# Kernel optimization log

Hardware: AMD Instinct MI355X
Metric: run time of the kernel (lower is better)

The kernel has to match this reference:

```python
import jax, jax.numpy as jnp
import numpy as np

B, S, D = 8, 2048, 512

def setup_inputs() -> dict:
    key = jax.random.key(0)
    ks = jax.random.split(key, 9)
    scale = 1.0 / np.sqrt(D)
    return {
        "x": jax.random.normal(ks[0], (B, S, D), dtype=jnp.float32),
        "attention_mask": jax.random.uniform(ks[1], (B, S), dtype=jnp.float32),
        "Wq": jax.random.normal(ks[2], (D, D), dtype=jnp.float32) * scale,
        "bq": jax.random.normal(ks[3], (D,), dtype=jnp.float32) * 0.01,
        "Wk": jax.random.normal(ks[4], (D, D), dtype=jnp.float32) * scale,
        "bk": jax.random.normal(ks[5], (D,), dtype=jnp.float32) * 0.01,
        "Wv": jax.random.normal(ks[6], (D, D), dtype=jnp.float32) * scale,
        "bv": jax.random.normal(ks[7], (D,), dtype=jnp.float32) * 0.01,
    }

def reference(x, attention_mask, Wq, bq, Wk, bk, Wv, bv):
    # Single-head self-attention, full O(S^2) scores as in the original.
    q = jnp.einsum('bsd,df->bsf', x, Wq) + bq  # [B,S,D]
    k = jnp.einsum('bsd,df->bsf', x, Wk) + bk
    v = jnp.einsum('bsd,df->bsf', x, Wv) + bv
    scores = jnp.einsum('bqd,bkd->bqk', q, k) / jnp.sqrt(jnp.float32(D))  # [B,S,S]
    attn = jax.nn.softmax(scores, axis=2)
    weighted = jnp.einsum('bqk,bkd->bqd', attn, v)  # [B,S,D]
    # mask applied multiplicatively to the output, per original code
    return weighted * attention_mask[:, :, None]
```

## Files before the change

### kernel.cpp

```cpp
#include <hip/hip_runtime.h>
#include <math.h>
#include <stdint.h>


typedef _Float16 f16x8 __attribute__((ext_vector_type(8)));
typedef _Float16 f16x4 __attribute__((ext_vector_type(4)));
typedef _Float16 f16x2 __attribute__((ext_vector_type(2)));
typedef float f32x4 __attribute__((ext_vector_type(4)));

__device__ __forceinline__ void async16(const _Float16* g, _Float16* l) {
    __builtin_amdgcn_global_load_lds(
        (const __attribute__((address_space(1))) unsigned int*)(uintptr_t)g,
        (__attribute__((address_space(3))) unsigned int*)(unsigned int)(uintptr_t)l,
        16, 0, 0);
}

__device__ __forceinline__ float frag_sum8(f16x8 v, float acc) {
#if __has_builtin(__builtin_amdgcn_fdot2)
    const f16x2 one2 = {(_Float16)1.f, (_Float16)1.f};
    const f16x2* p = (const f16x2*)&v;
    acc = __builtin_amdgcn_fdot2(p[0], one2, acc, false);
    acc = __builtin_amdgcn_fdot2(p[1], one2, acc, false);
    acc = __builtin_amdgcn_fdot2(p[2], one2, acc, false);
    acc = __builtin_amdgcn_fdot2(p[3], one2, acc, false);
#else
#pragma unroll
    for (int j = 0; j < 8; j++) acc += (float)v[j];
#endif
    return acc;
}

template <bool WITH_RS>
__device__ __forceinline__ void core8(
    const _Float16* __restrict__ A,
    const _Float16* __restrict__ B,
    int ld, int K, int row0, int col0,
    _Float16* sm, f32x4 acc[4][4], float rs[4])
{
    constexpr int CA = 32, L = 6, BUFH = 24576;
    const int tid = threadIdx.x, lane = tid & 63, wave = tid >> 6;
    const int wm = wave >> 1, wn = wave & 1;
    const int rc  = lane >> 3;
    const int swz = ((lane & 7) ^ rc) * 8;
    const int fr = lane & 15, q = lane >> 4, fx = fr & 7;

    const _Float16* g[L];
    int coff[L];
#pragma unroll
    for (int i = 0; i < L; i++) {
        int c = wave * L + i;
        const _Float16* base = (c < CA) ? A : B;
        int rr = (c < CA) ? (row0 + 8 * c) : (col0 + 8 * (c - CA));
        g[i]    = base + (size_t)(rr + rc) * ld + swz;
        coff[i] = c * 512;
    }

    const int NT = K >> 6;
#pragma unroll
    for (int i = 0; i < L; i++) async16(g[i], sm + coff[i]);
#pragma unroll
    for (int i = 0; i < L; i++) async16(g[i] + 64, sm + BUFH + coff[i]);
#pragma unroll
    for (int i = 0; i < L; i++) g[i] += 128;
    asm volatile("s_waitcnt vmcnt(6)" ::: "memory");
    asm volatile("" ::: "memory");
    __builtin_amdgcn_s_barrier();
    asm volatile("" ::: "memory");

#pragma unroll 2
    for (int t = 0; t < NT; ++t) {
        const _Float16* As = sm + (t & 1) * BUFH;
        const _Float16* Bs = As + CA * 512;
        f16x8 ah[2][2], b0[2][2], b1[2][2];

#pragma unroll
        for (int m = 0; m < 2; m++)
#pragma unroll
            for (int s = 0; s < 2; s++) {
                int ra = (wm * 4 + m) * 16 + fr;
                int kc = ((s * 4 + q) ^ fx) * 8;
                ah[m][s] = *(const f16x8*)&As[ra * 64 + kc];
            }
#pragma unroll
        for (int n = 0; n < 2; n++)
#pragma unroll
            for (int s = 0; s < 2; s++) {
                int rb = (wn * 4 + n) * 16 + fr;
                int kc = ((s * 4 + q) ^ fx) * 8;
                b0[n][s] = *(const f16x8*)&Bs[rb * 64 + kc];
            }
        if (WITH_RS) {
#pragma unroll
            for (int m = 0; m < 2; m++)
#pragma unroll
                for (int s = 0; s < 2; s++) rs[m] = frag_sum8(ah[m][s], rs[m]);
        }
        __builtin_amdgcn_s_setprio(1);
#pragma unroll
        for (int m = 0; m < 2; m++)
#pragma unroll
            for (int n = 0; n < 2; n++)
#pragma unroll
                for (int s = 0; s < 2; s++)
                    acc[m][n] = __builtin_amdgcn_mfma_f32_16x16x32_f16(
                        ah[m][s], b0[n][s], acc[m][n], 0, 0, 0);
        __builtin_amdgcn_s_setprio(0);

#pragma unroll
        for (int n = 0; n < 2; n++)
#pragma unroll
            for (int s = 0; s < 2; s++) {
                int rb = (wn * 4 + 2 + n) * 16 + fr;
                int kc = ((s * 4 + q) ^ fx) * 8;
                b1[n][s] = *(const f16x8*)&Bs[rb * 64 + kc];
            }
        __builtin_amdgcn_s_setprio(1);
#pragma unroll
        for (int m = 0; m < 2; m++)
#pragma unroll
            for (int n = 0; n < 2; n++)
#pragma unroll
                for (int s = 0; s < 2; s++)
                    acc[m][2 + n] = __builtin_amdgcn_mfma_f32_16x16x32_f16(
                        ah[m][s], b1[n][s], acc[m][2 + n], 0, 0, 0);
        __builtin_amdgcn_s_setprio(0);

#pragma unroll
        for (int m = 0; m < 2; m++)
#pragma unroll
            for (int s = 0; s < 2; s++) {
                int ra = (wm * 4 + 2 + m) * 16 + fr;
                int kc = ((s * 4 + q) ^ fx) * 8;
                ah[m][s] = *(const f16x8*)&As[ra * 64 + kc];
            }
        if (WITH_RS) {
#pragma unroll
            for (int m = 0; m < 2; m++)
#pragma unroll
                for (int s = 0; s < 2; s++) rs[2 + m] = frag_sum8(ah[m][s], rs[2 + m]);
        }
        __builtin_amdgcn_s_setprio(1);
#pragma unroll
        for (int m = 0; m < 2; m++)
#pragma unroll
            for (int n = 0; n < 2; n++)
#pragma unroll
                for (int s = 0; s < 2; s++)
                    acc[2 + m][2 + n] = __builtin_amdgcn_mfma_f32_16x16x32_f16(
                        ah[m][s], b1[n][s], acc[2 + m][2 + n], 0, 0, 0);
        __builtin_amdgcn_s_setprio(0);

        asm volatile("s_waitcnt lgkmcnt(0)" ::: "memory");
        asm volatile("" ::: "memory");
        __builtin_amdgcn_s_barrier();
        asm volatile("" ::: "memory");
        if (t + 2 < NT) {
            _Float16* db = sm + (t & 1) * BUFH;
#pragma unroll
            for (int i = 0; i < L; i++) async16(g[i], db + coff[i]);
#pragma unroll
            for (int i = 0; i < L; i++) g[i] += 64;
        }
        __builtin_amdgcn_s_setprio(1);
#pragma unroll
        for (int m = 0; m < 2; m++)
#pragma unroll
            for (int n = 0; n < 2; n++)
#pragma unroll
                for (int s = 0; s < 2; s++)
                    acc[2 + m][n] = __builtin_amdgcn_mfma_f32_16x16x32_f16(
                        ah[m][s], b0[n][s], acc[2 + m][n], 0, 0, 0);
        __builtin_amdgcn_s_setprio(0);
        if (t + 2 < NT) {
            asm volatile("s_waitcnt vmcnt(6)" ::: "memory");
        } else if (t + 1 < NT) {
            asm volatile("s_waitcnt vmcnt(0)" ::: "memory");
        }
        if (t + 1 < NT) {
            asm volatile("" ::: "memory");
            __builtin_amdgcn_s_barrier();
            asm volatile("" ::: "memory");
        }
    }
}

__global__ __launch_bounds__(256) void prep(
    const float* __restrict__ x,
    const float* __restrict__ Wq, const float* __restrict__ Wk,
    const float* __restrict__ Wv,
    _Float16* __restrict__ Xh,
    _Float16* __restrict__ WqT, _Float16* __restrict__ WkT,
    _Float16* __restrict__ WvT)
{
    const int bid = blockIdx.x;
    if (bid < 8192) {
        int i = (bid * 256 + threadIdx.x) * 4;
        float4 v = *(const float4*)(x + i);
        f16x4 h;
        h.x = (_Float16)v.x; h.y = (_Float16)v.y;
        h.z = (_Float16)v.z; h.w = (_Float16)v.w;
        *(f16x4*)&Xh[i] = h;
    } else {
        int t = bid - 8192;
        int z = t >> 10;
        const float* W = (z == 0) ? Wq : (z == 1) ? Wk : Wv;
        _Float16* Wt   = (z == 0) ? WqT : (z == 1) ? WkT : WvT;
        int idx = (t & 1023) * 256 + threadIdx.x;
        int n = idx >> 9, k = idx & 511;
        Wt[idx] = (_Float16)W[k * 512 + n];
    }
}

__global__ __launch_bounds__(512, 2) void proj_mfma(
    const _Float16* __restrict__ Xh,
    const _Float16* __restrict__ WqT, const float* __restrict__ bq,
    const _Float16* __restrict__ WkT, const float* __restrict__ bk,
    const _Float16* __restrict__ WvT, const float* __restrict__ bv,
    _Float16* __restrict__ Qh, _Float16* __restrict__ Kh,
    _Float16* __restrict__ Vt)
{
    __shared__ __align__(16) _Float16 smem[2 * 24576];

    const int z = blockIdx.z;
    f32x4 acc[4][4];
#pragma unroll
    for (int i = 0; i < 4; i++)
#pragma unroll
        for (int j = 0; j < 4; j++) acc[i][j] = (f32x4){0.f, 0.f, 0.f, 0.f};
    float rs_unused[4];

    const int lane = threadIdx.x & 63, wave = threadIdx.x >> 6;
    const int wm = wave >> 1, wn = wave & 1;
    const int er = (lane >> 4) * 4, ec = lane & 15;

    if (z < 2) {
        const _Float16* Wt = (z == 0) ? WqT : WkT;
        const float* bias  = (z == 0) ? bq : bk;
        _Float16* P        = (z == 0) ? Qh : Kh;
        const float sc     = (z == 0) ? 0.04419417382415922f : 1.0f;
        const int row0 = blockIdx.x * 256, col0 = blockIdx.y * 128;
        core8<false>(Xh, Wt, 512, 512, row0, col0, smem, acc, rs_unused);
#pragma unroll
        for (int mf = 0; mf < 4; mf++)
#pragma unroll
            for (int nf = 0; nf < 4; nf++) {
                int col = col0 + (wn * 4 + nf) * 16 + ec;
                float bb = bias[col];
#pragma unroll
                for (int r = 0; r < 4; r++) {
                    int row = row0 + (wm * 4 + mf) * 16 + er + r;
                    P[(size_t)row * 512 + col] = (_Float16)((acc[mf][nf][r] + bb) * sc);
                }
            }
    } else {
        const int idx = blockIdx.y * 64 + blockIdx.x;
        const int row0 = (idx >> 7) * 256;
        const int col0 = (idx & 127) * 128;
        core8<false>(WvT, Xh, 512, 512, row0, col0, smem, acc, rs_unused);
#pragma unroll
        for (int mf = 0; mf < 4; mf++)
#pragma unroll
            for (int nf = 0; nf < 4; nf++) {
                int col = col0 + (wn * 4 + nf) * 16 + ec;
                size_t obase = (size_t)(col >> 11) * (512 * 2048) + (col & 2047);
#pragma unroll
                for (int r = 0; r < 4; r++) {
                    int row = row0 + (wm * 4 + mf) * 16 + er + r;
                    Vt[obase + (size_t)row * 2048] = (_Float16)(acc[mf][nf][r] + bv[row]);
                }
            }
    }
}

__global__ __launch_bounds__(512, 2) void scores_mfma(
    const _Float16* __restrict__ Qh, const _Float16* __restrict__ Kh,
    _Float16* __restrict__ Sh)
{
    __shared__ __align__(16) _Float16 smem[2 * 24576];
    const int bid = blockIdx.x;
    const int b   = bid & 7;
    const int rem = bid >> 3;
    const int col0 = (rem & 15) * 128;
    const int row0 = (rem >> 4) * 256;

    const _Float16* A = Qh + (size_t)b * 2048 * 512;
    const _Float16* B = Kh + (size_t)b * 2048 * 512;
    _Float16* S = Sh + (size_t)b * 2048 * 2048;

    f32x4 acc[4][4];
#pragma unroll
    for (int i = 0; i < 4; i++)
#pragma unroll
        for (int j = 0; j < 4; j++) acc[i][j] = (f32x4){0.f, 0.f, 0.f, 0.f};
    float rs_unused[4];

    core8<false>(A, B, 512, 512, row0, col0, smem, acc, rs_unused);

    const int lane = threadIdx.x & 63, wave = threadIdx.x >> 6;
    const int wm = wave >> 1, wn = wave & 1;
    const int er = (lane >> 4) * 4, ec = lane & 15;
#pragma unroll
    for (int mf = 0; mf < 4; mf++)
#pragma unroll
        for (int nf = 0; nf < 4; nf++) {
            int col = col0 + (wn * 4 + nf) * 16 + ec;
#pragma unroll
            for (int r = 0; r < 4; r++) {
                int row = row0 + (wm * 4 + mf) * 16 + er + r;
                S[(size_t)row * 2048 + col] = (_Float16)__expf(acc[mf][nf][r]);
            }
        }
}

__global__ __launch_bounds__(512, 2) void av_mfma(
    const _Float16* __restrict__ Sh, const _Float16* __restrict__ Vt,
    const float* __restrict__ mask, float* __restrict__ out)
{
    __shared__ __align__(16) _Float16 smem[2 * 24576];
    const int bid = blockIdx.x;
    const int b   = bid & 7;
    const int rem = bid >> 3;
    const int col0 = (rem & 3) * 128;
    const int row0 = (rem >> 2) * 256;

    const _Float16* A = Sh + (size_t)b * 2048 * 2048;
    const _Float16* B = Vt + (size_t)b * 512 * 2048;
    float* O = out + (size_t)b * 2048 * 512;
    const float* mk = mask + (size_t)b * 2048;

    f32x4 acc[4][4];
#pragma unroll
    for (int i = 0; i < 4; i++)
#pragma unroll
        for (int j = 0; j < 4; j++) acc[i][j] = (f32x4){0.f, 0.f, 0.f, 0.f};
    float rs[4] = {0.f, 0.f, 0.f, 0.f};

    core8<true>(A, B, 2048, 2048, row0, col0, smem, acc, rs);

    const int lane = threadIdx.x & 63, wave = threadIdx.x >> 6;
    const int wm = wave >> 1, wn = wave & 1;
    const int er = (lane >> 4) * 4, ec = lane & 15;

#pragma unroll
    for (int mf = 0; mf < 4; mf++) {
        rs[mf] += __shfl_xor(rs[mf], 16, 64);
        rs[mf] += __shfl_xor(rs[mf], 32, 64);
    }
    __syncthreads();
    float* l_s = (float*)smem;
    if (wn == 0 && lane < 16) {
#pragma unroll
        for (int mf = 0; mf < 4; mf++) l_s[wm * 64 + mf * 16 + lane] = rs[mf];
    }
    __syncthreads();

#pragma unroll
    for (int mf = 0; mf < 4; mf++)
#pragma unroll
        for (int r = 0; r < 4; r++) {
            int lrow = wm * 64 + mf * 16 + er + r;
            int row = row0 + lrow;
            float s = mk[row] / l_s[lrow];
#pragma unroll
            for (int nf = 0; nf < 4; nf++) {
                int col = col0 + (wn * 4 + nf) * 16 + ec;
                O[(size_t)row * 512 + col] = acc[mf][nf][r] * s;
            }
        }
}

extern "C" void kernel_launch(void* const* d_in, const int* in_sizes, int n_in,
                              void* d_out, int out_size, void* d_ws, size_t ws_size,
                              hipStream_t stream) {
    const float* x    = (const float*)d_in[0];
    const float* mask = (const float*)d_in[1];
    const float* Wq   = (const float*)d_in[2];
    const float* bq   = (const float*)d_in[3];
    const float* Wk   = (const float*)d_in[4];
    const float* bk   = (const float*)d_in[5];
    const float* Wv   = (const float*)d_in[6];
    const float* bv   = (const float*)d_in[7];
    float* out = (float*)d_out;

    const size_t BSD = (size_t)8 * 2048 * 512;
    _Float16* base = (_Float16*)d_ws;
    _Float16* Qh  = base;
    _Float16* Kh  = Qh + BSD;
    _Float16* Vt  = Kh + BSD;
    _Float16* WqT = Vt + BSD;
    _Float16* WkT = WqT + 512 * 512;
    _Float16* WvT = WkT + 512 * 512;
    _Float16* Xh  = WvT + 512 * 512;
    _Float16* Sh  = Xh;

    prep<<<dim3(8192 + 3 * 1024), dim3(256), 0, stream>>>(
        x, Wq, Wk, Wv, Xh, WqT, WkT, WvT);
    proj_mfma<<<dim3(64, 4, 3), dim3(512), 0, stream>>>(
        Xh, WqT, bq, WkT, bk, WvT, bv, Qh, Kh, Vt);
    scores_mfma<<<dim3(1024), dim3(512), 0, stream>>>(Qh, Kh, Sh);
    av_mfma<<<dim3(256), dim3(512), 0, stream>>>(Sh, Vt, mask, out);
}
```

Before: 217.2 us.

## Use 256x256 block tiles for projection and scores GEMMs with staggered prefetch

```diff
diff --git a/kernel.cpp b/kernel.cpp
--- a/kernel.cpp
+++ b/kernel.cpp
@@ -30,157 +30,252 @@
     return acc;
 }
 
-template <bool WITH_RS>
-__device__ __forceinline__ void core8(
-    const _Float16* __restrict__ A,
-    const _Float16* __restrict__ B,
-    int ld, int K, int row0, int col0,
-    _Float16* sm, f32x4 acc[4][4], float rs[4])
-{
-    constexpr int CA = 32, L = 6, BUFH = 24576;
+#define MFMA16(a, b, c) __builtin_amdgcn_mfma_f32_16x16x32_f16(a, b, c, 0, 0, 0)
+#define BAR() __builtin_amdgcn_s_barrier()
+#define LGKM0() asm volatile("s_waitcnt lgkmcnt(0)" ::: "memory")
+
+template <int NT>
+__device__ __forceinline__ void core256(
+    const _Float16* __restrict__ A, const _Float16* __restrict__ B,
+    int ld, int row0, int col0, _Float16* sm, f32x4 acc[8][4])
+{
+    const int tid = threadIdx.x, lane = tid & 63, wave = tid >> 6;
+    const int wm = wave >> 2, wn = wave & 3;
+    const int rc = lane >> 3;
+    const int swz = ((lane & 7) ^ rc) * 8;
+    const int fr = lane & 15, q = lane >> 4, fx = fr & 7;
+    const size_t laneoff = (size_t)rc * ld + swz;
+
+    const _Float16* gc[8];
+    int lc[8];
+    {
+        const int i0 = wave * 2, i1 = i0 + 1;
+        const int a0 = (i0 < 8) ? i0 : i0 + 8;
+        const int a1 = (i1 < 8) ? i1 : i1 + 8;
+        const int b0 = (i0 & 3) + (i0 >> 2) * 8;
+        const int b1 = (i1 & 3) + (i1 >> 2) * 8;
+        gc[0] = A + (size_t)(row0 + 8 * a0) * ld + laneoff;       lc[0] = a0 * 512;
+        gc[1] = A + (size_t)(row0 + 8 * a1) * ld + laneoff;       lc[1] = a1 * 512;
+        gc[2] = B + (size_t)(col0 + 8 * b0) * ld + laneoff;       lc[2] = 16384 + b0 * 512;
+        gc[3] = B + (size_t)(col0 + 8 * b1) * ld + laneoff;       lc[3] = 16384 + b1 * 512;
+        gc[4] = B + (size_t)(col0 + 8 * (b0 + 4)) * ld + laneoff; lc[4] = 16384 + (b0 + 4) * 512;
+        gc[5] = B + (size_t)(col0 + 8 * (b1 + 4)) * ld + laneoff; lc[5] = 16384 + (b1 + 4) * 512;
+        gc[6] = A + (size_t)(row0 + 8 * (a0 + 8)) * ld + laneoff; lc[6] = (a0 + 8) * 512;
+        gc[7] = A + (size_t)(row0 + 8 * (a1 + 8)) * ld + laneoff; lc[7] = (a1 + 8) * 512;
+    }
+
+#pragma unroll
+    for (int i = 0; i < 8; i++) async16(gc[i], sm + lc[i]);
+#pragma unroll
+    for (int i = 0; i < 8; i++) async16(gc[i] + 64, sm + 32768 + lc[i]);
+    asm volatile("s_waitcnt vmcnt(8)" ::: "memory");
+    BAR();
+
+#pragma unroll 2
+    for (int t = 0; t < NT; ++t) {
+        const _Float16* As = sm + (t & 1) * 32768;
+        const _Float16* Bs = As + 16384;
+        _Float16* stg = sm + (t & 1) * 32768;
+        const int k2 = (t + 2) * 64;
+        const bool pf = (t + 2 < NT);
+        f16x8 a0f[4][2], a1f[4][2], b0f[2][2], b1f[2][2];
+
+#pragma unroll
+        for (int m = 0; m < 4; m++)
+#pragma unroll
+            for (int s = 0; s < 2; s++) {
+                int ra = wm * 128 + m * 16 + fr;
+                a0f[m][s] = *(const f16x8*)&As[ra * 64 + (((s * 4 + q) ^ fx) * 8)];
+            }
+#pragma unroll
+        for (int n = 0; n < 2; n++)
+#pragma unroll
+            for (int s = 0; s < 2; s++) {
+                int rb = wn * 64 + n * 16 + fr;
+                b0f[n][s] = *(const f16x8*)&Bs[rb * 64 + (((s * 4 + q) ^ fx) * 8)];
+            }
+        BAR(); LGKM0();
+        __builtin_amdgcn_s_setprio(1);
+#pragma unroll
+        for (int s = 0; s < 2; s++)
+#pragma unroll
+            for (int m = 0; m < 4; m++)
+#pragma unroll
+                for (int n = 0; n < 2; n++)
+                    acc[m][n] = MFMA16(a0f[m][s], b0f[n][s], acc[m][n]);
+        __builtin_amdgcn_s_setprio(0);
+        BAR();
+
+#pragma unroll
+        for (int n = 0; n < 2; n++)
+#pragma unroll
+            for (int s = 0; s < 2; s++) {
+                int rb = wn * 64 + (2 + n) * 16 + fr;
+                b1f[n][s] = *(const f16x8*)&Bs[rb * 64 + (((s * 4 + q) ^ fx) * 8)];
+            }
+        if (pf) {
+#pragma unroll
+            for (int i = 0; i < 4; i++) async16(gc[i] + k2, stg + lc[i]);
+        }
+        BAR(); LGKM0();
+        __builtin_amdgcn_s_setprio(1);
+#pragma unroll
+        for (int s = 0; s < 2; s++)
+#pragma unroll
+            for (int m = 0; m < 4; m++)
+#pragma unroll
+                for (int n = 0; n < 2; n++)
+                    acc[m][2 + n] = MFMA16(a0f[m][s], b1f[n][s], acc[m][2 + n]);
+        __builtin_amdgcn_s_setprio(0);
+        BAR();
+
+#pragma unroll
+        for (int m = 0; m < 4; m++)
+#pragma unroll
+            for (int s = 0; s < 2; s++) {
+                int ra = wm * 128 + (4 + m) * 16 + fr;
+                a1f[m][s] = *(const f16x8*)&As[ra * 64 + (((s * 4 + q) ^ fx) * 8)];
+            }
+        if (pf) {
+            async16(gc[4] + k2, stg + lc[4]);
+            async16(gc[5] + k2, stg + lc[5]);
+        }
+        BAR(); LGKM0();
+        __builtin_amdgcn_s_setprio(1);
+#pragma unroll
+        for (int s = 0; s < 2; s++)
+#pragma unroll
+            for (int m = 0; m < 4; m++)
+#pragma unroll
+                for (int n = 0; n < 2; n++)
+                    acc[4 + m][2 + n] = MFMA16(a1f[m][s], b1f[n][s], acc[4 + m][2 + n]);
+        __builtin_amdgcn_s_setprio(0);
+        BAR();
+
+        if (pf) {
+            async16(gc[6] + k2, stg + lc[6]);
+            async16(gc[7] + k2, stg + lc[7]);
+            asm volatile("s_waitcnt vmcnt(8)" ::: "memory");
+        } else {
+            asm volatile("s_waitcnt vmcnt(0)" ::: "memory");
+        }
+        __builtin_amdgcn_s_setprio(1);
+#pragma unroll
+        for (int s = 0; s < 2; s++)
+#pragma unroll
+            for (int m = 0; m < 4; m++)
+#pragma unroll
+                for (int n = 0; n < 2; n++)
+                    acc[4 + m][n] = MFMA16(a1f[m][s], b0f[n][s], acc[4 + m][n]);
+        __builtin_amdgcn_s_setprio(0);
+        BAR();
+    }
+}
+
+template <int NT, bool WITH_RS>
+__device__ __forceinline__ void core128(
+    const _Float16* __restrict__ A, const _Float16* __restrict__ B,
+    int ld, int row0, int col0, _Float16* sm, f32x4 acc[4][4], float rs[4])
+{
     const int tid = threadIdx.x, lane = tid & 63, wave = tid >> 6;
     const int wm = wave >> 1, wn = wave & 1;
-    const int rc  = lane >> 3;
+    const int rc = lane >> 3;
     const int swz = ((lane & 7) ^ rc) * 8;
     const int fr = lane & 15, q = lane >> 4, fx = fr & 7;
-
-    const _Float16* g[L];
-    int coff[L];
-#pragma unroll
-    for (int i = 0; i < L; i++) {
-        int c = wave * L + i;
-        const _Float16* base = (c < CA) ? A : B;
-        int rr = (c < CA) ? (row0 + 8 * c) : (col0 + 8 * (c - CA));
-        g[i]    = base + (size_t)(rr + rc) * ld + swz;
-        coff[i] = c * 512;
-    }
-
-    const int NT = K >> 6;
-#pragma unroll
-    for (int i = 0; i < L; i++) async16(g[i], sm + coff[i]);
-#pragma unroll
-    for (int i = 0; i < L; i++) async16(g[i] + 64, sm + BUFH + coff[i]);
-#pragma unroll
-    for (int i = 0; i < L; i++) g[i] += 128;
-    asm volatile("s_waitcnt vmcnt(6)" ::: "memory");
-    asm volatile("" ::: "memory");
-    __builtin_amdgcn_s_barrier();
-    asm volatile("" ::: "memory");
+    const size_t laneoff = (size_t)rc * ld + swz;
+
+    const _Float16* gA[4]; int lA[4];
+#pragma unroll
+    for (int i = 0; i < 4; i++) {
+        int c = wave * 4 + i;
+        gA[i] = A + (size_t)(row0 + 8 * c) * ld + laneoff;
+        lA[i] = c * 512;
+    }
+    const int cb0 = (wave & 3) + (wave >> 2) * 8;
+    const _Float16* gB0 = B + (size_t)(col0 + 8 * cb0) * ld + laneoff;
+    const _Float16* gB1 = B + (size_t)(col0 + 8 * (cb0 + 4)) * ld + laneoff;
+    const int lB0 = 16384 + cb0 * 512;
+    const int lB1 = 16384 + (cb0 + 4) * 512;
+
+#pragma unroll
+    for (int i = 0; i < 4; i++) async16(gA[i], sm + lA[i]);
+    async16(gB0, sm + lB0);
+    async16(gB1, sm + lB1);
+#pragma unroll
+    for (int i = 0; i < 4; i++) async16(gA[i] + 64, sm + 24576 + lA[i]);
+    async16(gB0 + 64, sm + 24576 + lB0);
+    asm volatile("s_waitcnt vmcnt(5)" ::: "memory");
+    BAR();
 
 #pragma unroll 2
     for (int t = 0; t < NT; ++t) {
-        const _Float16* As = sm + (t & 1) * BUFH;
-        const _Float16* Bs = As + CA * 512;
-        f16x8 ah[2][2], b0[2][2], b1[2][2];
-
-#pragma unroll
-        for (int m = 0; m < 2; m++)
-#pragma unroll
-            for (int s = 0; s < 2; s++) {
-                int ra = (wm * 4 + m) * 16 + fr;
-                int kc = ((s * 4 + q) ^ fx) * 8;
-                ah[m][s] = *(const f16x8*)&As[ra * 64 + kc];
+        const _Float16* As = sm + (t & 1) * 24576;
+        const _Float16* Bs = As + 16384;
+        _Float16* stg  = sm + (t & 1) * 24576;
+        _Float16* stgn = sm + ((t + 1) & 1) * 24576;
+        const int k1 = (t + 1) * 64;
+        const int k2 = (t + 2) * 64;
+        f16x8 af[4][2], b0f[2][2], b1f[2][2];
+
+#pragma unroll
+        for (int m = 0; m < 4; m++)
+#pragma unroll
+            for (int s = 0; s < 2; s++) {
+                int ra = wm * 64 + m * 16 + fr;
+                af[m][s] = *(const f16x8*)&As[ra * 64 + (((s * 4 + q) ^ fx) * 8)];
             }
 #pragma unroll
         for (int n = 0; n < 2; n++)
 #pragma unroll
             for (int s = 0; s < 2; s++) {
-                int rb = (wn * 4 + n) * 16 + fr;
-                int kc = ((s * 4 + q) ^ fx) * 8;
-                b0[n][s] = *(const f16x8*)&Bs[rb * 64 + kc];
-            }
+                int rb = wn * 64 + n * 16 + fr;
+                b0f[n][s] = *(const f16x8*)&Bs[rb * 64 + (((s * 4 + q) ^ fx) * 8)];
+            }
+        if (t + 1 < NT) async16(gB1 + k1, stgn + lB1);
+        BAR(); LGKM0();
         if (WITH_RS) {
 #pragma unroll
-            for (int m = 0; m < 2; m++)
-#pragma unroll
-                for (int s = 0; s < 2; s++) rs[m] = frag_sum8(ah[m][s], rs[m]);
-        }
-        __builtin_amdgcn_s_setprio(1);
-#pragma unroll
-        for (int m = 0; m < 2; m++)
-#pragma unroll
-            for (int n = 0; n < 2; n++)
-#pragma unroll
-                for (int s = 0; s < 2; s++)
-                    acc[m][n] = __builtin_amdgcn_mfma_f32_16x16x32_f16(
-                        ah[m][s], b0[n][s], acc[m][n], 0, 0, 0);
-        __builtin_amdgcn_s_setprio(0);
+            for (int m = 0; m < 4; m++)
+#pragma unroll
+                for (int s = 0; s < 2; s++) rs[m] = frag_sum8(af[m][s], rs[m]);
+        }
+        __builtin_amdgcn_s_setprio(1);
+#pragma unroll
+        for (int s = 0; s < 2; s++)
+#pragma unroll
+            for (int m = 0; m < 4; m++)
+#pragma unroll
+                for (int n = 0; n < 2; n++)
+                    acc[m][n] = MFMA16(af[m][s], b0f[n][s], acc[m][n]);
+        __builtin_amdgcn_s_setprio(0);
+        BAR();
 
 #pragma unroll
         for (int n = 0; n < 2; n++)
 #pragma unroll
             for (int s = 0; s < 2; s++) {
-                int rb = (wn * 4 + 2 + n) * 16 + fr;
-                int kc = ((s * 4 + q) ^ fx) * 8;
-                b1[n][s] = *(const f16x8*)&Bs[rb * 64 + kc];
-            }
-        __builtin_amdgcn_s_setprio(1);
-#pragma unroll
-        for (int m = 0; m < 2; m++)
-#pragma unroll
-            for (int n = 0; n < 2; n++)
-#pragma unroll
-                for (int s = 0; s < 2; s++)
-                    acc[m][2 + n] = __builtin_amdgcn_mfma_f32_16x16x32_f16(
-                        ah[m][s], b1[n][s], acc[m][2 + n], 0, 0, 0);
-        __builtin_amdgcn_s_setprio(0);
-
-#pragma unroll
-        for (int m = 0; m < 2; m++)
-#pragma unroll
-            for (int s = 0; s < 2; s++) {
-                int ra = (wm * 4 + 2 + m) * 16 + fr;
-                int kc = ((s * 4 + q) ^ fx) * 8;
-                ah[m][s] = *(const f16x8*)&As[ra * 64 + kc];
-            }
-        if (WITH_RS) {
-#pragma unroll
-            for (int m = 0; m < 2; m++)
-#pragma unroll
-                for (int s = 0; s < 2; s++) rs[2 + m] = frag_sum8(ah[m][s], rs[2 + m]);
-        }
-        __builtin_amdgcn_s_setprio(1);
-#pragma unroll
-        for (int m = 0; m < 2; m++)
-#pragma unroll
-            for (int n = 0; n < 2; n++)
-#pragma unroll
-                for (int s = 0; s < 2; s++)
-                    acc[2 + m][2 + n] = __builtin_amdgcn_mfma_f32_16x16x32_f16(
-                        ah[m][s], b1[n][s], acc[2 + m][2 + n], 0, 0, 0);
-        __builtin_amdgcn_s_setprio(0);
-
-        asm volatile("s_waitcnt lgkmcnt(0)" ::: "memory");
-        asm volatile("" ::: "memory");
-        __builtin_amdgcn_s_barrier();
-        asm volatile("" ::: "memory");
+                int rb = wn * 64 + (2 + n) * 16 + fr;
+                b1f[n][s] = *(const f16x8*)&Bs[rb * 64 + (((s * 4 + q) ^ fx) * 8)];
+            }
         if (t + 2 < NT) {
-            _Float16* db = sm + (t & 1) * BUFH;
-#pragma unroll
-            for (int i = 0; i < L; i++) async16(g[i], db + coff[i]);
-#pragma unroll
-            for (int i = 0; i < L; i++) g[i] += 64;
-        }
-        __builtin_amdgcn_s_setprio(1);
-#pragma unroll
-        for (int m = 0; m < 2; m++)
-#pragma unroll
-            for (int n = 0; n < 2; n++)
-#pragma unroll
-                for (int s = 0; s < 2; s++)
-                    acc[2 + m][n] = __builtin_amdgcn_mfma_f32_16x16x32_f16(
-                        ah[m][s], b0[n][s], acc[2 + m][n], 0, 0, 0);
-        __builtin_amdgcn_s_setprio(0);
-        if (t + 2 < NT) {
-            asm volatile("s_waitcnt vmcnt(6)" ::: "memory");
-        } else if (t + 1 < NT) {
+#pragma unroll
+            for (int i = 0; i < 4; i++) async16(gA[i] + k2, stg + lA[i]);
+            async16(gB0 + k2, stg + lB0);
+            asm volatile("s_waitcnt vmcnt(5)" ::: "memory");
+        } else {
             asm volatile("s_waitcnt vmcnt(0)" ::: "memory");
         }
-        if (t + 1 < NT) {
-            asm volatile("" ::: "memory");
-            __builtin_amdgcn_s_barrier();
-            asm volatile("" ::: "memory");
-        }
+        BAR(); LGKM0();
+        __builtin_amdgcn_s_setprio(1);
+#pragma unroll
+        for (int s = 0; s < 2; s++)
+#pragma unroll
+            for (int m = 0; m < 4; m++)
+#pragma unroll
+                for (int n = 0; n < 2; n++)
+                    acc[m][2 + n] = MFMA16(af[m][s], b1f[n][s], acc[m][2 + n]);
+        __builtin_amdgcn_s_setprio(0);
+        BAR();
     }
 }
 
@@ -219,18 +314,16 @@
     _Float16* __restrict__ Qh, _Float16* __restrict__ Kh,
     _Float16* __restrict__ Vt)
 {
-    __shared__ __align__(16) _Float16 smem[2 * 24576];
-
+    __shared__ __align__(16) _Float16 smem[2 * 32768];
     const int z = blockIdx.z;
-    f32x4 acc[4][4];
-#pragma unroll
-    for (int i = 0; i < 4; i++)
+    f32x4 acc[8][4];
+#pragma unroll
+    for (int i = 0; i < 8; i++)
 #pragma unroll
         for (int j = 0; j < 4; j++) acc[i][j] = (f32x4){0.f, 0.f, 0.f, 0.f};
-    float rs_unused[4];
 
     const int lane = threadIdx.x & 63, wave = threadIdx.x >> 6;
-    const int wm = wave >> 1, wn = wave & 1;
+    const int wm = wave >> 2, wn = wave & 3;
     const int er = (lane >> 4) * 4, ec = lane & 15;
 
     if (z < 2) {
@@ -238,34 +331,33 @@
         const float* bias  = (z == 0) ? bq : bk;
         _Float16* P        = (z == 0) ? Qh : Kh;
         const float sc     = (z == 0) ? 0.04419417382415922f : 1.0f;
-        const int row0 = blockIdx.x * 256, col0 = blockIdx.y * 128;
-        core8<false>(Xh, Wt, 512, 512, row0, col0, smem, acc, rs_unused);
-#pragma unroll
-        for (int mf = 0; mf < 4; mf++)
+        const int row0 = blockIdx.x * 256, col0 = blockIdx.y * 256;
+        core256<8>(Xh, Wt, 512, row0, col0, smem, acc);
+#pragma unroll
+        for (int mf = 0; mf < 8; mf++)
 #pragma unroll
             for (int nf = 0; nf < 4; nf++) {
-                int col = col0 + (wn * 4 + nf) * 16 + ec;
+                int col = col0 + wn * 64 + nf * 16 + ec;
                 float bb = bias[col];
 #pragma unroll
                 for (int r = 0; r < 4; r++) {
-                    int row = row0 + (wm * 4 + mf) * 16 + er + r;
+                    int row = row0 + wm * 128 + mf * 16 + er + r;
                     P[(size_t)row * 512 + col] = (_Float16)((acc[mf][nf][r] + bb) * sc);
                 }
             }
     } else {
-        const int idx = blockIdx.y * 64 + blockIdx.x;
-        const int row0 = (idx >> 7) * 256;
-        const int col0 = (idx & 127) * 128;
-        core8<false>(WvT, Xh, 512, 512, row0, col0, smem, acc, rs_unused);
-#pragma unroll
-        for (int mf = 0; mf < 4; mf++)
+        const int row0 = blockIdx.y * 256;
+        const int col0 = blockIdx.x * 256;
+        core256<8>(WvT, Xh, 512, row0, col0, smem, acc);
+#pragma unroll
+        for (int mf = 0; mf < 8; mf++)
 #pragma unroll
             for (int nf = 0; nf < 4; nf++) {
-                int col = col0 + (wn * 4 + nf) * 16 + ec;
+                int col = col0 + wn * 64 + nf * 16 + ec;
                 size_t obase = (size_t)(col >> 11) * (512 * 2048) + (col & 2047);
 #pragma unroll
                 for (int r = 0; r < 4; r++) {
-                    int row = row0 + (wm * 4 + mf) * 16 + er + r;
+                    int row = row0 + wm * 128 + mf * 16 + er + r;
                     Vt[obase + (size_t)row * 2048] = (_Float16)(acc[mf][nf][r] + bv[row]);
                 }
             }
@@ -276,37 +368,36 @@
     const _Float16* __restrict__ Qh, const _Float16* __restrict__ Kh,
     _Float16* __restrict__ Sh)
 {
-    __shared__ __align__(16) _Float16 smem[2 * 24576];
+    __shared__ __align__(16) _Float16 smem[2 * 32768];
     const int bid = blockIdx.x;
     const int b   = bid & 7;
     const int rem = bid >> 3;
-    const int col0 = (rem & 15) * 128;
-    const int row0 = (rem >> 4) * 256;
+    const int col0 = (rem & 7) * 256;
+    const int row0 = (rem >> 3) * 256;
 
     const _Float16* A = Qh + (size_t)b * 2048 * 512;
     const _Float16* B = Kh + (size_t)b * 2048 * 512;
     _Float16* S = Sh + (size_t)b * 2048 * 2048;
 
-    f32x4 acc[4][4];
-#pragma unroll
-    for (int i = 0; i < 4; i++)
+    f32x4 acc[8][4];
+#pragma unroll
+    for (int i = 0; i < 8; i++)
 #pragma unroll
         for (int j = 0; j < 4; j++) acc[i][j] = (f32x4){0.f, 0.f, 0.f, 0.f};
-    float rs_unused[4];
-
-    core8<false>(A, B, 512, 512, row0, col0, smem, acc, rs_unused);
+
+    core256<8>(A, B, 512, row0, col0, smem, acc);
 
     const int lane = threadIdx.x & 63, wave = threadIdx.x >> 6;
-    const int wm = wave >> 1, wn = wave & 1;
+    const int wm = wave >> 2, wn = wave & 3;
     const int er = (lane >> 4) * 4, ec = lane & 15;
 #pragma unroll
-    for (int mf = 0; mf < 4; mf++)
+    for (int mf = 0; mf < 8; mf++)
 #pragma unroll
         for (int nf = 0; nf < 4; nf++) {
-            int col = col0 + (wn * 4 + nf) * 16 + ec;
+            int col = col0 + wn * 64 + nf * 16 + ec;
 #pragma unroll
             for (int r = 0; r < 4; r++) {
-                int row = row0 + (wm * 4 + mf) * 16 + er + r;
+                int row = row0 + wm * 128 + mf * 16 + er + r;
                 S[(size_t)row * 2048 + col] = (_Float16)__expf(acc[mf][nf][r]);
             }
         }
@@ -335,7 +426,7 @@
         for (int j = 0; j < 4; j++) acc[i][j] = (f32x4){0.f, 0.f, 0.f, 0.f};
     float rs[4] = {0.f, 0.f, 0.f, 0.f};
 
-    core8<true>(A, B, 2048, 2048, row0, col0, smem, acc, rs);
+    core128<32, true>(A, B, 2048, row0, col0, smem, acc, rs);
 
     const int lane = threadIdx.x & 63, wave = threadIdx.x >> 6;
     const int wm = wave >> 1, wn = wave & 1;
@@ -363,7 +454,7 @@
             float s = mk[row] / l_s[lrow];
 #pragma unroll
             for (int nf = 0; nf < 4; nf++) {
-                int col = col0 + (wn * 4 + nf) * 16 + ec;
+                int col = col0 + wn * 64 + nf * 16 + ec;
                 O[(size_t)row * 512 + col] = acc[mf][nf][r] * s;
             }
         }
@@ -395,8 +486,8 @@
 
     prep<<<dim3(8192 + 3 * 1024), dim3(256), 0, stream>>>(
         x, Wq, Wk, Wv, Xh, WqT, WkT, WvT);
-    proj_mfma<<<dim3(64, 4, 3), dim3(512), 0, stream>>>(
+    proj_mfma<<<dim3(64, 2, 3), dim3(512), 0, stream>>>(
         Xh, WqT, bq, WkT, bk, WvT, bv, Qh, Kh, Vt);
-    scores_mfma<<<dim3(1024), dim3(512), 0, stream>>>(Qh, Kh, Sh);
+    scores_mfma<<<dim3(512), dim3(512), 0, stream>>>(Qh, Kh, Sh);
     av_mfma<<<dim3(256), dim3(512), 0, stream>>>(Sh, Vt, mask, out);
 }
```

New measurement: 221.4 us. No clear change (+2.0%).
